# Optimization experiments

Hardware: AMD Instinct MI355X
Metric: run time of the kernel (lower is better)

The kernel has to match this reference:

```python
import jax, jax.numpy as jnp
import numpy as np
import math

B, S, D, H, FF, L = 8, 1024, 1024, 8, 4096, 2
DK = D // H
NEG = -1e32
EPS = 1e-5


def _cosine_pe(seq_len, d_model):
    pos = jnp.arange(seq_len, dtype=jnp.float32)[:, None]
    div = jnp.exp(jnp.arange(0, d_model, 2, dtype=jnp.float32) * (-(math.log(10000.0) / d_model)))
    pe = jnp.zeros((seq_len, d_model), dtype=jnp.float32)
    pe = pe.at[:, 0::2].set(jnp.sin(pos * div))
    pe = pe.at[:, 1::2].set(jnp.cos(pos * div))
    return pe


def setup_inputs() -> dict:
    key = jax.random.key(0)
    ks = jax.random.split(key, 12)
    sc = 0.02
    g = lambda k, shape: (jax.random.normal(k, shape, jnp.float32) * sc)
    return {
        "q_embed": jax.random.normal(ks[0], (B, S, D), jnp.float32),
        "qa_embed": jax.random.normal(ks[1], (B, S, D), jnp.float32),
        "pos_emb": _cosine_pe(S, D),
        "Wk": g(ks[2], (L, D, D)), "bk": jnp.zeros((L, D), jnp.float32),
        "Wv": g(ks[3], (L, D, D)), "bv": jnp.zeros((L, D), jnp.float32),
        "Wo": g(ks[4], (L, D, D)), "bo": jnp.zeros((L, D), jnp.float32),
        "ln1_g": jnp.ones((L, D), jnp.float32), "ln1_b": jnp.zeros((L, D), jnp.float32),
        "W1": g(ks[5], (L, FF, D)), "b1": jnp.zeros((L, FF), jnp.float32),
        "W2": g(ks[6], (L, D, FF)), "b2": jnp.zeros((L, D), jnp.float32),
        "ln2_g": jnp.ones((L, D), jnp.float32), "ln2_b": jnp.zeros((L, D), jnp.float32),
    }


def _layernorm(x, g, b):
    m = jnp.mean(x, axis=-1, keepdims=True)
    v = jnp.mean(jnp.square(x - m), axis=-1, keepdims=True)
    return (x - m) * jax.lax.rsqrt(v + EPS) * g + b


def _mha(x, y, Wk, bk, Wv, bv, Wo, bo, allow):
    # kq_same=1: q and k both come from k_linear applied to x (query==key input)
    k = (jnp.einsum('bsd,od->bso', x, Wk) + bk).reshape(B, S, H, DK).transpose(0, 2, 1, 3)
    q = k  # identical projection and identical input
    v = (jnp.einsum('bsd,od->bso', y, Wv) + bv).reshape(B, S, H, DK).transpose(0, 2, 1, 3)
    scores = jnp.einsum('bhqd,bhkd->bhqk', q, k) / math.sqrt(DK)
    scores = jnp.where(allow, scores, NEG)  # masked_fill(mask==0, -1e32)
    attn = jax.nn.softmax(scores, axis=-1)
    attn = attn.at[:, :, 0, :].set(0.0)  # zero_pad: first query row zeroed
    out = jnp.einsum('bhqk,bhkd->bhqd', attn, v)
    out = out.transpose(0, 2, 1, 3).reshape(B, S, D)
    return jnp.einsum('bsd,od->bso', out, Wo) + bo


def reference(q_embed, qa_embed, pos_emb, Wk, bk, Wv, bv, Wo, bo,
              ln1_g, ln1_b, W1, b1, W2, b2, ln2_g, ln2_b):
    x = q_embed + pos_emb[None]
    y = qa_embed + pos_emb[None]
    # strictly-lower-triangular allowed positions (triu(k=0)==0)
    allow = jnp.tril(jnp.ones((S, S), dtype=bool), -1)[None, None]
    for l in range(L):
        q2 = _mha(x, x, y, Wk[l], bk[l], Wv[l], bv[l], Wo[l], bo[l], allow) if False else _mha(x, y, Wk[l], bk[l], Wv[l], bv[l], Wo[l], bo[l], allow)
        x = _layernorm(x + q2, ln1_g[l], ln1_b[l])
        ff = jnp.einsum('bsf,df->bsd', jax.nn.relu(jnp.einsum('bsd,fd->bsf', x, W1[l]) + b1[l]), W2[l]) + b2[l]
        x = _layernorm(x + ff, ln2_g[l], ln2_b[l])
    return x
```

## Files before the change

### kernel.cpp

```cpp
#include <hip/hip_runtime.h>
#include <hip/hip_bf16.h>
#include <cstdint>
#include <cstddef>

#define B_  8
#define S_  1024
#define D_  1024
#define H_  8
#define FF_ 4096
#define L_  2
#define DK_ 128

typedef __bf16 bf16x8 __attribute__((ext_vector_type(8)));
typedef float  f32x4  __attribute__((ext_vector_type(4)));

__device__ __forceinline__ unsigned short f2bf(float f) {
    union { float f; uint32_t u; } v; v.f = f;
    uint32_t r = v.u + 0x7fffu + ((v.u >> 16) & 1u);
    return (unsigned short)(r >> 16);
}
__device__ __forceinline__ float bf2f(unsigned short u) {
    union { uint32_t u; float f; } v; v.u = ((uint32_t)u) << 16; return v.f;
}

__global__ __launch_bounds__(256) void init_xy(
    const float* __restrict__ qe, const float* __restrict__ qa,
    const float* __restrict__ pe,
    unsigned short* __restrict__ xb, unsigned short* __restrict__ yb)
{
    int i = (blockIdx.x * 256 + threadIdx.x) * 4;
    int pi = i & (S_ * D_ - 1);
    float4 q = *(const float4*)(qe + i);
    float4 a = *(const float4*)(qa + i);
    float4 p = *(const float4*)(pe + pi);
    ushort4 xo; xo.x = f2bf(q.x + p.x); xo.y = f2bf(q.y + p.y);
    xo.z = f2bf(q.z + p.z); xo.w = f2bf(q.w + p.w);
    ushort4 yo; yo.x = f2bf(a.x + p.x); yo.y = f2bf(a.y + p.y);
    yo.z = f2bf(a.z + p.z); yo.w = f2bf(a.w + p.w);
    *(ushort4*)(xb + i) = xo;
    *(ushort4*)(yb + i) = yo;
}

__global__ __launch_bounds__(256) void cvt_bf16(
    const float* __restrict__ in, unsigned short* __restrict__ out)
{
    int i = (blockIdx.x * 256 + threadIdx.x) * 4;
    float4 f = *(const float4*)(in + i);
    ushort4 o; o.x = f2bf(f.x); o.y = f2bf(f.y); o.z = f2bf(f.z); o.w = f2bf(f.w);
    *(ushort4*)(out + i) = o;
}

template<bool RELU, int OMODE>
__global__ __launch_bounds__(256) void gemm_bt(
    const unsigned short* __restrict__ A, const unsigned short* __restrict__ W,
    const float* __restrict__ bias, void* __restrict__ Cout,
    int M, int N, int K)
{
    __shared__ unsigned short sA[2][128][64];
    __shared__ unsigned short sW[2][128][64];

    const int tid  = threadIdx.x;
    const int lane = tid & 63;
    const int w    = tid >> 6;
    const int l16  = lane & 15;
    const int quad = lane >> 4;
    const int m0 = blockIdx.y * 128;
    const int n0 = blockIdx.x * 128;
    const int rw = (w >> 1) * 64;
    const int cw = (w & 1) * 64;

    const int srow   = lane >> 3;
    const int schunk = lane & 7;

    auto stage = [&](int k0, int buf) {
        #pragma unroll
        for (int i = 0; i < 4; ++i) {
            int r0  = w * 32 + i * 8;
            int row = r0 + srow;
            int gc  = schunk ^ (row & 7);
            const unsigned short* ga = A + (size_t)(m0 + row) * K + k0 + gc * 8;
            const unsigned short* gw = W + (size_t)(n0 + row) * K + k0 + gc * 8;
            __builtin_amdgcn_global_load_lds(
                (const __attribute__((address_space(1))) unsigned int*)ga,
                (__attribute__((address_space(3))) unsigned int*)&sA[buf][r0][0], 16, 0, 0);
            __builtin_amdgcn_global_load_lds(
                (const __attribute__((address_space(1))) unsigned int*)gw,
                (__attribute__((address_space(3))) unsigned int*)&sW[buf][r0][0], 16, 0, 0);
        }
    };

    f32x4 acc[4][4] = {};
    const int NK = K >> 6;
    int cur = 0;
    stage(0, 0);

    for (int kt = 0; kt < NK; ++kt) {
        __syncthreads();
        if (kt + 1 < NK) stage((kt + 1) << 6, cur ^ 1);

        #pragma unroll
        for (int ks = 0; ks < 2; ++ks) {
            bf16x8 af[4], wf[4];
            #pragma unroll
            for (int t = 0; t < 4; ++t) {
                int arow = rw + t * 16 + l16;
                int achk = (ks * 4 + quad) ^ (arow & 7);
                af[t] = *(const bf16x8*)&sA[cur][arow][achk * 8];
                int wrow = cw + t * 16 + l16;
                int wchk = (ks * 4 + quad) ^ (wrow & 7);
                wf[t] = *(const bf16x8*)&sW[cur][wrow][wchk * 8];
            }
            #pragma unroll
            for (int it = 0; it < 4; ++it)
                #pragma unroll
                for (int jt = 0; jt < 4; ++jt)
                    acc[it][jt] = __builtin_amdgcn_mfma_f32_16x16x32_bf16(
                        af[it], wf[jt], acc[it][jt], 0, 0, 0);
        }
        cur ^= 1;
    }

    #pragma unroll
    for (int it = 0; it < 4; ++it)
        #pragma unroll
        for (int jt = 0; jt < 4; ++jt) {
            int row = m0 + rw + it * 16 + quad * 4;
            int col = n0 + cw + jt * 16 + l16;
            float bcol = bias[col];
            float v[4];
            #pragma unroll
            for (int r = 0; r < 4; ++r) {
                v[r] = acc[it][jt][r] + bcol;
                if (RELU) v[r] = fmaxf(v[r], 0.0f);
            }
            if (OMODE == 1) {
                #pragma unroll
                for (int r = 0; r < 4; ++r)
                    ((unsigned short*)Cout)[(size_t)(row + r) * N + col] = f2bf(v[r]);
            } else {
                int key = row & (S_ - 1);
                int bb  = row >> 10;
                int hh  = col >> 7, dim = col & (DK_ - 1);
                unsigned short* dst = (unsigned short*)Cout
                    + ((size_t)(bb * H_ + hh) * DK_ + dim) * S_ + key;
                ushort4 o4; o4.x = f2bf(v[0]); o4.y = f2bf(v[1]);
                o4.z = f2bf(v[2]); o4.w = f2bf(v[3]);
                *(ushort4*)dst = o4;
            }
        }
}

__global__ __launch_bounds__(256) void attn_mfma(
    const unsigned short* __restrict__ Kbuf, const unsigned short* __restrict__ Vtbuf,
    unsigned short* __restrict__ Obuf)
{
    __shared__ unsigned short sK[2][64][128];
    __shared__ unsigned short sVt[2][128][64];
    __shared__ unsigned short sP[4][16][72];

    const int tid  = threadIdx.x;
    const int lane = tid & 63;
    const int w    = tid >> 6;
    const int l16  = lane & 15;
    const int quad = lane >> 4;
    const int pa   = blockIdx.x;
    const int bh   = blockIdx.y;
    const int b    = bh >> 3, h = bh & 7;
    const unsigned short* KB  = Kbuf  + ((size_t)b * S_) * D_ + h * DK_;
    const unsigned short* VTB = Vtbuf + (size_t)bh * DK_ * S_;

    const float scale = 0.08838834764831845f;

    auto stage = [&](int kt, int buf) {
        #pragma unroll
        for (int i = 0; i < 4; ++i) {
            int r0  = w * 16 + i * 4;
            int row = r0 + (lane >> 4);
            int c   = (lane & 15) ^ (row & 15);
            const unsigned short* g = KB + (size_t)(kt * 64 + row) * D_ + c * 8;
            __builtin_amdgcn_global_load_lds(
                (const __attribute__((address_space(1))) unsigned int*)g,
                (__attribute__((address_space(3))) unsigned int*)&sK[buf][r0][0], 16, 0, 0);
        }
        #pragma unroll
        for (int i = 0; i < 4; ++i) {
            int r0  = w * 32 + i * 8;
            int row = r0 + (lane >> 3);
            int c   = (lane & 7) ^ (row & 7);
            const unsigned short* g = VTB + (size_t)row * S_ + kt * 64 + c * 8;
            __builtin_amdgcn_global_load_lds(
                (const __attribute__((address_space(1))) unsigned int*)g,
                (__attribute__((address_space(3))) unsigned int*)&sVt[buf][r0][0], 16, 0, 0);
        }
    };

    #pragma unroll
    for (int half = 0; half < 2; ++half) {
        const int qt = half == 0 ? (15 - pa) : pa;
        const int q0 = qt * 64;

        bf16x8 qf[4];
        {
            const unsigned short* qrow = KB + (size_t)(q0 + w * 16 + l16) * D_ + quad * 8;
            #pragma unroll
            for (int ks = 0; ks < 4; ++ks)
                qf[ks] = *(const bf16x8*)(qrow + ks * 32);
        }

        f32x4 Oacc[8] = {};
        float m_run[4] = {-1e30f, -1e30f, -1e30f, -1e30f};
        float l_run[4] = {};

        int cur = 0;
        stage(0, cur);

        for (int kt = 0; kt <= qt; ++kt) {
            __syncthreads();
            if (kt < qt) stage(kt + 1, cur ^ 1);

            f32x4 sacc[4];
            #pragma unroll
            for (int nt = 0; nt < 4; ++nt) {
                f32x4 a = {};
                #pragma unroll
                for (int ks = 0; ks < 4; ++ks) {
                    int kr = nt * 16 + l16;
                    int p  = (ks * 4 + quad) ^ (kr & 15);
                    bf16x8 kf = *(const bf16x8*)&sK[cur][kr][p * 8];
                    a = __builtin_amdgcn_mfma_f32_16x16x32_bf16(qf[ks], kf, a, 0, 0, 0);
                }
                sacc[nt] = a;
            }

            const bool diag = (kt == qt);
            #pragma unroll
            for (int nt = 0; nt < 4; ++nt)
                #pragma unroll
                for (int r = 0; r < 4; ++r) {
                    float v = sacc[nt][r] * scale;
                    if (diag) {
                        int nidx = nt * 16 + l16;
                        int midx = w * 16 + quad * 4 + r;
                        if (nidx >= midx) v = -1e30f;
                    }
                    sacc[nt][r] = v;
                }

            float alpha[4];
            #pragma unroll
            for (int r = 0; r < 4; ++r) {
                float mx = fmaxf(fmaxf(sacc[0][r], sacc[1][r]), fmaxf(sacc[2][r], sacc[3][r]));
                mx = fmaxf(mx, __shfl_xor(mx, 1));
                mx = fmaxf(mx, __shfl_xor(mx, 2));
                mx = fmaxf(mx, __shfl_xor(mx, 4));
                mx = fmaxf(mx, __shfl_xor(mx, 8));
                float mn = fmaxf(m_run[r], mx);
                alpha[r] = __expf(m_run[r] - mn);
                m_run[r] = mn;
            }
            #pragma unroll
            for (int r = 0; r < 4; ++r) {
                float rs = 0.0f;
                #pragma unroll
                for (int nt = 0; nt < 4; ++nt) {
                    float e = __expf(sacc[nt][r] - m_run[r]);
                    sacc[nt][r] = e;
                    rs += e;
                }
                rs += __shfl_xor(rs, 1);
                rs += __shfl_xor(rs, 2);
                rs += __shfl_xor(rs, 4);
                rs += __shfl_xor(rs, 8);
                l_run[r] = l_run[r] * alpha[r] + rs;
            }
            #pragma unroll
            for (int o = 0; o < 8; ++o)
                #pragma unroll
                for (int r = 0; r < 4; ++r)
                    Oacc[o][r] *= alpha[r];

            #pragma unroll
            for (int nt = 0; nt < 4; ++nt)
                #pragma unroll
                for (int r = 0; r < 4; ++r)
                    sP[w][quad * 4 + r][nt * 16 + l16] = f2bf(sacc[nt][r]);

            bf16x8 pf[2];
            #pragma unroll
            for (int ks = 0; ks < 2; ++ks)
                pf[ks] = *(const bf16x8*)&sP[w][l16][ks * 32 + quad * 8];
            #pragma unroll
            for (int nt = 0; nt < 8; ++nt) {
                #pragma unroll
                for (int ks = 0; ks < 2; ++ks) {
                    int vr = nt * 16 + l16;
                    int p  = (ks * 4 + quad) ^ (vr & 7);
                    bf16x8 vf = *(const bf16x8*)&sVt[cur][vr][p * 8];
                    Oacc[nt] = __builtin_amdgcn_mfma_f32_16x16x32_bf16(pf[ks], vf, Oacc[nt], 0, 0, 0);
                }
            }
            cur ^= 1;
        }

        float inv[4];
        #pragma unroll
        for (int r = 0; r < 4; ++r) {
            int m = q0 + w * 16 + quad * 4 + r;
            inv[r] = (l_run[r] > 0.0f && m != 0) ? 1.0f / l_run[r] : 0.0f;
        }
        #pragma unroll
        for (int nt = 0; nt < 8; ++nt)
            #pragma unroll
            for (int r = 0; r < 4; ++r) {
                int m = q0 + w * 16 + quad * 4 + r;
                Obuf[((size_t)b * S_ + m) * D_ + h * DK_ + nt * 16 + l16] =
                    f2bf(Oacc[nt][r] * inv[r]);
            }
    }
}

template<bool FINAL>
__global__ __launch_bounds__(256) void ln_res(
    const unsigned short* __restrict__ xin, const unsigned short* __restrict__ delta,
    const float* __restrict__ g, const float* __restrict__ bta,
    unsigned short* __restrict__ xbout, float* __restrict__ fout)
{
    __shared__ float red1[4], red2[4];
    const int row = blockIdx.x;
    const int tid = threadIdx.x;
    const int c = tid * 4;
    ushort4 xu = *(const ushort4*)(xin + (size_t)row * D_ + c);
    ushort4 du = *(const ushort4*)(delta + (size_t)row * D_ + c);
    float t0 = bf2f(xu.x) + bf2f(du.x), t1 = bf2f(xu.y) + bf2f(du.y);
    float t2 = bf2f(xu.z) + bf2f(du.z), t3 = bf2f(xu.w) + bf2f(du.w);

    float s = t0 + t1 + t2 + t3;
    #pragma unroll
    for (int off = 32; off > 0; off >>= 1) s += __shfl_down(s, off);
    if ((tid & 63) == 0) red1[tid >> 6] = s;
    __syncthreads();
    float mean = (red1[0] + red1[1] + red1[2] + red1[3]) * (1.0f / 1024.0f);

    float e0 = t0 - mean, e1 = t1 - mean, e2 = t2 - mean, e3 = t3 - mean;
    float ss = e0 * e0 + e1 * e1 + e2 * e2 + e3 * e3;
    #pragma unroll
    for (int off = 32; off > 0; off >>= 1) ss += __shfl_down(ss, off);
    if ((tid & 63) == 0) red2[tid >> 6] = ss;
    __syncthreads();
    float var = (red2[0] + red2[1] + red2[2] + red2[3]) * (1.0f / 1024.0f);
    float rstd = rsqrtf(var + 1e-5f);

    float4 gv = *(const float4*)(g + c);
    float4 bv = *(const float4*)(bta + c);
    float o0 = e0 * rstd * gv.x + bv.x;
    float o1 = e1 * rstd * gv.y + bv.y;
    float o2 = e2 * rstd * gv.z + bv.z;
    float o3 = e3 * rstd * gv.w + bv.w;
    if (FINAL) {
        *(float4*)(fout + (size_t)row * D_ + c) = make_float4(o0, o1, o2, o3);
    } else {
        ushort4 ob; ob.x = f2bf(o0); ob.y = f2bf(o1); ob.z = f2bf(o2); ob.w = f2bf(o3);
        *(ushort4*)(xbout + (size_t)row * D_ + c) = ob;
    }
}

extern "C" void kernel_launch(void* const* d_in, const int* in_sizes, int n_in,
                              void* d_out, int out_size, void* d_ws, size_t ws_size,
                              hipStream_t stream)
{
    const float* qe   = (const float*)d_in[0];
    const float* qa   = (const float*)d_in[1];
    const float* pe   = (const float*)d_in[2];
    const float* Wk   = (const float*)d_in[3];
    const float* bk   = (const float*)d_in[4];
    const float* Wv   = (const float*)d_in[5];
    const float* bv   = (const float*)d_in[6];
    const float* Wo   = (const float*)d_in[7];
    const float* bo   = (const float*)d_in[8];
    const float* ln1g = (const float*)d_in[9];
    const float* ln1b = (const float*)d_in[10];
    const float* W1   = (const float*)d_in[11];
    const float* b1   = (const float*)d_in[12];
    const float* W2   = (const float*)d_in[13];
    const float* b2   = (const float*)d_in[14];
    const float* ln2g = (const float*)d_in[15];
    const float* ln2b = (const float*)d_in[16];

    const size_t BSD = (size_t)B_ * S_ * D_;
    const size_t BSF = (size_t)B_ * S_ * FF_;
    const size_t WDD = (size_t)D_ * D_;
    const size_t WFD = (size_t)FF_ * D_;

    char* p = (char*)d_ws;
    auto take = [&](size_t bytes) { char* r = p; p += (bytes + 255) & ~255ULL; return r; };
    unsigned short* xb    = (unsigned short*)take(BSD * 2);
    unsigned short* yb    = (unsigned short*)take(BSD * 2);
    unsigned short* delta = (unsigned short*)take(BSD * 2);
    char*           uni   = take(BSF * 2);
    unsigned short* Kb    = (unsigned short*)uni;
    unsigned short* Vt    = Kb + BSD;
    unsigned short* attnb = Vt + BSD;
    unsigned short* hb    = (unsigned short*)uni;
    unsigned short* wslot = (unsigned short*)take(WFD * 2);

    init_xy<<<(int)(BSD / 4 / 256), 256, 0, stream>>>(qe, qa, pe, xb, yb);

    const int M = B_ * S_;
    for (int l = 0; l < L_; ++l) {
        cvt_bf16<<<(int)(WDD / 1024), 256, 0, stream>>>(Wk + l * WDD, wslot);
        gemm_bt<false, 1><<<dim3(D_ / 128, M / 128), 256, 0, stream>>>(
            xb, wslot, bk + l * D_, Kb, M, D_, D_);
        cvt_bf16<<<(int)(WDD / 1024), 256, 0, stream>>>(Wv + l * WDD, wslot);
        gemm_bt<false, 2><<<dim3(D_ / 128, M / 128), 256, 0, stream>>>(
            yb, wslot, bv + l * D_, Vt, M, D_, D_);
        attn_mfma<<<dim3(8, B_ * H_), 256, 0, stream>>>(Kb, Vt, attnb);
        cvt_bf16<<<(int)(WDD / 1024), 256, 0, stream>>>(Wo + l * WDD, wslot);
        gemm_bt<false, 1><<<dim3(D_ / 128, M / 128), 256, 0, stream>>>(
            attnb, wslot, bo + l * D_, delta, M, D_, D_);
        ln_res<false><<<M, 256, 0, stream>>>(xb, delta, ln1g + l * D_, ln1b + l * D_, xb, nullptr);
        cvt_bf16<<<(int)(WFD / 1024), 256, 0, stream>>>(W1 + l * WFD, wslot);
        gemm_bt<true, 1><<<dim3(FF_ / 128, M / 128), 256, 0, stream>>>(
            xb, wslot, b1 + l * FF_, hb, M, FF_, D_);
        cvt_bf16<<<(int)(WFD / 1024), 256, 0, stream>>>(W2 + l * WFD, wslot);
        gemm_bt<false, 1><<<dim3(D_ / 128, M / 128), 256, 0, stream>>>(
            hb, wslot, b2 + l * D_, delta, M, D_, FF_);
        if (l == L_ - 1)
            ln_res<true><<<M, 256, 0, stream>>>(xb, delta, ln2g + l * D_, ln2b + l * D_,
                                               nullptr, (float*)d_out);
        else
            ln_res<false><<<M, 256, 0, stream>>>(xb, delta, ln2g + l * D_, ln2b + l * D_,
                                                xb, nullptr);
    }
}
```

Before: 846.9 us.

## Add 256x256-tile 8-wave GEMM with LDS-direct loads for FFN up-projection

Adds a new GEMM kernel with 256x256 output tiles, 512 threads (8 waves), XOR-swizzled shared memory filled by global_load_lds, double buffering with the next tile's loads interleaved between MFMA phases, s_setprio around MFMA bursts, and a grouped (XCD-aware) block remap. It replaces the 128x128 GEMM for the W1 up-projection only. The aim is more reuse per loaded byte and better overlap of global loads with matrix math. In exchange it uses 128 KB of LDS per block and a large accumulator array, which can limit occupancy or cause register spills, and the write-out is uncoalesced per-element bf16 stores.

```diff
diff --git a/kernel.cpp b/kernel.cpp
--- a/kernel.cpp
+++ b/kernel.cpp
@@ -146,6 +146,163 @@
                 ushort4 o4; o4.x = f2bf(v[0]); o4.y = f2bf(v[1]);
                 o4.z = f2bf(v[2]); o4.w = f2bf(v[3]);
                 *(ushort4*)dst = o4;
+            }
+        }
+}
+
+template<bool RELU>
+__global__ __launch_bounds__(512, 2) void gemm_bt8(
+    const unsigned short* __restrict__ A, const unsigned short* __restrict__ W,
+    const float* __restrict__ bias, unsigned short* __restrict__ Cout,
+    int M, int N, int K)
+{
+    __shared__ unsigned short sA[2][256][64];
+    __shared__ unsigned short sB[2][256][64];
+
+    const int tid  = threadIdx.x;
+    const int lane = tid & 63;
+    const int w    = tid >> 6;
+    const int l16  = lane & 15;
+    const int quad = lane >> 4;
+    const int wr   = w >> 2;
+    const int wc   = w & 3;
+
+    const int nwg = gridDim.x * gridDim.y;
+    const int bid = blockIdx.y * gridDim.x + blockIdx.x;
+    const int sb  = (bid & 7) * (nwg >> 3) + (bid >> 3);
+    const int m0  = (sb / gridDim.x) * 256;
+    const int n0  = (sb % gridDim.x) * 256;
+
+    const int srow8 = lane >> 3;
+    const int schk  = (lane & 7) ^ srow8;
+
+    auto stA = [&](int i, int buf, int k0) {
+        int r0 = i * 64 + w * 8;
+        const unsigned short* g = A + (size_t)(m0 + r0 + srow8) * K + k0 + schk * 8;
+        __builtin_amdgcn_global_load_lds(
+            (const __attribute__((address_space(1))) unsigned int*)g,
+            (__attribute__((address_space(3))) unsigned int*)&sA[buf][r0][0], 16, 0, 0);
+    };
+    auto stB = [&](int i, int buf, int k0) {
+        int r0 = i * 64 + w * 8;
+        const unsigned short* g = W + (size_t)(n0 + r0 + srow8) * K + k0 + schk * 8;
+        __builtin_amdgcn_global_load_lds(
+            (const __attribute__((address_space(1))) unsigned int*)g,
+            (__attribute__((address_space(3))) unsigned int*)&sB[buf][r0][0], 16, 0, 0);
+    };
+    auto rdA = [&](int buf, int t, int ks) {
+        int row = wr * 128 + t * 16 + l16;
+        int chk = (ks * 4 + quad) ^ (row & 7);
+        return *(const bf16x8*)&sA[buf][row][chk * 8];
+    };
+    auto rdB = [&](int buf, int j, int ks) {
+        int row = wc * 64 + j * 16 + l16;
+        int chk = (ks * 4 + quad) ^ (row & 7);
+        return *(const bf16x8*)&sB[buf][row][chk * 8];
+    };
+
+    f32x4 acc[8][4] = {};
+    const int NK = K >> 6;
+    int cur = 0;
+
+    stB(0, 0, 0); stB(1, 0, 0); stB(2, 0, 0); stB(3, 0, 0);
+    stA(0, 0, 0); stA(2, 0, 0); stA(1, 0, 0); stA(3, 0, 0);
+    asm volatile("s_waitcnt vmcnt(2)\n\ts_barrier" ::: "memory");
+
+    for (int kt = 0; kt < NK; ++kt) {
+        const bool pref = (kt + 1 < NK);
+        const int  k1   = (kt + 1) << 6;
+        const int  nb   = cur ^ 1;
+        bf16x8 bfr[2][4];
+        bf16x8 a0, a1, a2, a3;
+
+        #pragma unroll
+        for (int ks = 0; ks < 2; ++ks)
+            #pragma unroll
+            for (int j = 0; j < 4; ++j) bfr[ks][j] = rdB(cur, j, ks);
+        a0 = rdA(cur, 0, 0); a1 = rdA(cur, 0, 1);
+        a2 = rdA(cur, 1, 0); a3 = rdA(cur, 1, 1);
+        if (pref) { stB(0, nb, k1); stB(1, nb, k1); }
+        __builtin_amdgcn_s_setprio(1);
+        #pragma unroll
+        for (int j = 0; j < 4; ++j) {
+            acc[0][j] = __builtin_amdgcn_mfma_f32_16x16x32_bf16(a0, bfr[0][j], acc[0][j], 0, 0, 0);
+            acc[1][j] = __builtin_amdgcn_mfma_f32_16x16x32_bf16(a2, bfr[0][j], acc[1][j], 0, 0, 0);
+        }
+        #pragma unroll
+        for (int j = 0; j < 4; ++j) {
+            acc[0][j] = __builtin_amdgcn_mfma_f32_16x16x32_bf16(a1, bfr[1][j], acc[0][j], 0, 0, 0);
+            acc[1][j] = __builtin_amdgcn_mfma_f32_16x16x32_bf16(a3, bfr[1][j], acc[1][j], 0, 0, 0);
+        }
+        __builtin_amdgcn_s_setprio(0);
+        asm volatile("s_barrier" ::: "memory");
+
+        a0 = rdA(cur, 2, 0); a1 = rdA(cur, 2, 1);
+        a2 = rdA(cur, 3, 0); a3 = rdA(cur, 3, 1);
+        if (pref) { stB(2, nb, k1); stB(3, nb, k1); }
+        __builtin_amdgcn_s_setprio(1);
+        #pragma unroll
+        for (int j = 0; j < 4; ++j) {
+            acc[2][j] = __builtin_amdgcn_mfma_f32_16x16x32_bf16(a0, bfr[0][j], acc[2][j], 0, 0, 0);
+            acc[3][j] = __builtin_amdgcn_mfma_f32_16x16x32_bf16(a2, bfr[0][j], acc[3][j], 0, 0, 0);
+        }
+        #pragma unroll
+        for (int j = 0; j < 4; ++j) {
+            acc[2][j] = __builtin_amdgcn_mfma_f32_16x16x32_bf16(a1, bfr[1][j], acc[2][j], 0, 0, 0);
+            acc[3][j] = __builtin_amdgcn_mfma_f32_16x16x32_bf16(a3, bfr[1][j], acc[3][j], 0, 0, 0);
+        }
+        __builtin_amdgcn_s_setprio(0);
+        if (pref) asm volatile("s_waitcnt vmcnt(4)\n\ts_barrier" ::: "memory");
+        else      asm volatile("s_waitcnt vmcnt(0)\n\ts_barrier" ::: "memory");
+
+        a0 = rdA(cur, 4, 0); a1 = rdA(cur, 4, 1);
+        a2 = rdA(cur, 5, 0); a3 = rdA(cur, 5, 1);
+        if (pref) { stA(0, nb, k1); stA(2, nb, k1); }
+        __builtin_amdgcn_s_setprio(1);
+        #pragma unroll
+        for (int j = 0; j < 4; ++j) {
+            acc[4][j] = __builtin_amdgcn_mfma_f32_16x16x32_bf16(a0, bfr[0][j], acc[4][j], 0, 0, 0);
+            acc[5][j] = __builtin_amdgcn_mfma_f32_16x16x32_bf16(a2, bfr[0][j], acc[5][j], 0, 0, 0);
+        }
+        #pragma unroll
+        for (int j = 0; j < 4; ++j) {
+            acc[4][j] = __builtin_amdgcn_mfma_f32_16x16x32_bf16(a1, bfr[1][j], acc[4][j], 0, 0, 0);
+            acc[5][j] = __builtin_amdgcn_mfma_f32_16x16x32_bf16(a3, bfr[1][j], acc[5][j], 0, 0, 0);
+        }
+        __builtin_amdgcn_s_setprio(0);
+        asm volatile("s_barrier" ::: "memory");
+
+        a0 = rdA(cur, 6, 0); a1 = rdA(cur, 6, 1);
+        a2 = rdA(cur, 7, 0); a3 = rdA(cur, 7, 1);
+        if (pref) { stA(1, nb, k1); stA(3, nb, k1); }
+        __builtin_amdgcn_s_setprio(1);
+        #pragma unroll
+        for (int j = 0; j < 4; ++j) {
+            acc[6][j] = __builtin_amdgcn_mfma_f32_16x16x32_bf16(a0, bfr[0][j], acc[6][j], 0, 0, 0);
+            acc[7][j] = __builtin_amdgcn_mfma_f32_16x16x32_bf16(a2, bfr[0][j], acc[7][j], 0, 0, 0);
+        }
+        #pragma unroll
+        for (int j = 0; j < 4; ++j) {
+            acc[6][j] = __builtin_amdgcn_mfma_f32_16x16x32_bf16(a1, bfr[1][j], acc[6][j], 0, 0, 0);
+            acc[7][j] = __builtin_amdgcn_mfma_f32_16x16x32_bf16(a3, bfr[1][j], acc[7][j], 0, 0, 0);
+        }
+        __builtin_amdgcn_s_setprio(0);
+        asm volatile("s_waitcnt vmcnt(2)\n\ts_barrier" ::: "memory");
+        cur = nb;
+    }
+
+    #pragma unroll
+    for (int t = 0; t < 8; ++t)
+        #pragma unroll
+        for (int j = 0; j < 4; ++j) {
+            int row = m0 + wr * 128 + t * 16 + quad * 4;
+            int col = n0 + wc * 64 + j * 16 + l16;
+            float bcol = bias[col];
+            #pragma unroll
+            for (int r = 0; r < 4; ++r) {
+                float v = acc[t][j][r] + bcol;
+                if (RELU) v = fmaxf(v, 0.0f);
+                Cout[(size_t)(row + r) * N + col] = f2bf(v);
             }
         }
 }
@@ -419,7 +576,7 @@
             attnb, wslot, bo + l * D_, delta, M, D_, D_);
         ln_res<false><<<M, 256, 0, stream>>>(xb, delta, ln1g + l * D_, ln1b + l * D_, xb, nullptr);
         cvt_bf16<<<(int)(WFD / 1024), 256, 0, stream>>>(W1 + l * WFD, wslot);
-        gemm_bt<true, 1><<<dim3(FF_ / 128, M / 128), 256, 0, stream>>>(
+        gemm_bt8<true><<<dim3(FF_ / 256, M / 256), 512, 0, stream>>>(
             xb, wslot, b1 + l * FF_, hb, M, FF_, D_);
         cvt_bf16<<<(int)(WFD / 1024), 256, 0, stream>>>(W2 + l * WFD, wslot);
         gemm_bt<false, 1><<<dim3(D_ / 128, M / 128), 256, 0, stream>>>(
```

Measured after the change: 830.1 us. 2.0% less time.
